# Kernel tuning notes

Hardware: AMD Instinct MI355X
Metric: run time of the kernel (lower is better)

## Reference

```python
import jax, jax.numpy as jnp
import numpy as np

U, I, D = 100000, 100000, 64
B, T = 16384, 1_638_400
R = 5  # rating levels 1..5


def setup_inputs() -> dict:
    key = jax.random.key(0)
    ks = jax.random.split(key, 8)
    return {
        "user_idx": jax.random.randint(ks[0], (B,), 0, U, dtype=jnp.int32),
        "item_idx": jax.random.randint(ks[1], (B,), 0, I, dtype=jnp.int32),
        "flat_items": jax.random.randint(ks[2], (T,), 0, I, dtype=jnp.int32),
        "seg_ids": jnp.sort(jax.random.randint(ks[3], (T,), 0, B * R, dtype=jnp.int32)),
        "user_emb": (jax.random.uniform(ks[4], (U, D), dtype=jnp.float32) - 0.5) * 0.01,
        "item_emb": (jax.random.uniform(ks[5], (I, D), dtype=jnp.float32) - 0.5) * 0.01,
        "Mr": (jax.random.uniform(ks[6], (I, D), dtype=jnp.float32) - 0.5) * 0.01,
        "user_bias": jnp.zeros((U,), dtype=jnp.float32),
        "item_bias": jnp.zeros((I,), dtype=jnp.float32),
        "global_avg": jnp.float32(3.5),
    }


def reference(user_idx, item_idx, flat_items, seg_ids, user_emb, item_emb, Mr, user_bias, item_bias, global_avg):
    num_seg = B * R  # segment = sample_i * 5 + (rating - 1)
    # Original torch code does Mr_ik(rate_dict).sum() -> scalar over ALL dims,
    # then broadcasts that scalar onto the latent_dim vector UuMpc[i].
    row_sum = Mr[flat_items].sum(axis=-1)  # [T] per-item full-row sum
    # Emulate `rate_dict.remove(item_idx[i])`: mask out the target item of this sample.
    match = flat_items == item_idx[seg_ids // R]  # [T]
    contrib = jnp.where(match, 0.0, row_sum)
    seg_sum = jax.ops.segment_sum(contrib, seg_ids, num_segments=num_seg)  # [B*5]
    cnt = jax.ops.segment_sum(jnp.where(match, 0.0, 1.0), seg_ids, num_segments=num_seg)
    per_seg = jnp.where(cnt > 0, seg_sum / jnp.sqrt(jnp.maximum(cnt, 1.0)), 0.0)
    uu_mpc = per_seg.reshape(B, R).sum(axis=-1)  # [B] scalar per sample
    user_vec = user_emb[user_idx] + uu_mpc[:, None]  # broadcast scalar over latent dim
    item_vec = item_emb[item_idx]
    rui = (user_vec * item_vec).sum(axis=-1) + user_bias[user_idx] + item_bias[item_idx] + global_avg
    return jnp.clip(rui, 1.0, 5.0)
```

## Files before the change

kernel.cpp:

```cpp
#include <hip/hip_runtime.h>

#define U_N 100000
#define I_N 100000
#define D_N 64
#define B_N 16384
#define T_N 1638400
#define R_N 5
#define NSEG (B_N * R_N)
#define CHUNK 16

__global__ void rowsum_kernel(const float* __restrict__ Mr, float* __restrict__ rowsum) {
    int wave = (blockIdx.x * blockDim.x + threadIdx.x) >> 6;
    int lane = threadIdx.x & 63;
    if (wave >= I_N) return;
    float v = Mr[(long)wave * D_N + lane];
    #pragma unroll
    for (int off = 32; off >= 1; off >>= 1) v += __shfl_xor(v, off, 64);
    if (lane == 0) rowsum[wave] = v;
}

__global__ void seg_kernel(const int* __restrict__ flat_items,
                           const int* __restrict__ seg_ids,
                           const int* __restrict__ item_idx,
                           const float* __restrict__ rowsum,
                           float* __restrict__ seg_sum,
                           int* __restrict__ seg_cnt) {
    int tid = blockIdx.x * blockDim.x + threadIdx.x;
    long base = (long)tid * CHUNK;
    if (base >= T_N) return;

    const int4* fi4 = (const int4*)(flat_items + base);
    const int4* si4 = (const int4*)(seg_ids + base);

    int cur_seg = -1;
    float acc = 0.f;
    int cnt = 0;

    #pragma unroll
    for (int c = 0; c < CHUNK / 4; ++c) {
        int4 fi = fi4[c];
        int4 si = si4[c];
        int f[4] = {fi.x, fi.y, fi.z, fi.w};
        int s[4] = {si.x, si.y, si.z, si.w};
        #pragma unroll
        for (int j = 0; j < 4; ++j) {
            int sg = s[j];
            if (sg != cur_seg) {
                if (cnt > 0) {
                    atomicAdd(&seg_sum[cur_seg], acc);
                    atomicAdd(&seg_cnt[cur_seg], cnt);
                }
                cur_seg = sg; acc = 0.f; cnt = 0;
            }
            int it = f[j];
            if (it != item_idx[sg / R_N]) {
                acc += rowsum[it];
                cnt += 1;
            }
        }
    }
    if (cnt > 0) {
        atomicAdd(&seg_sum[cur_seg], acc);
        atomicAdd(&seg_cnt[cur_seg], cnt);
    }
}

__global__ void final_kernel(const int* __restrict__ user_idx,
                             const int* __restrict__ item_idx,
                             const float* __restrict__ user_emb,
                             const float* __restrict__ item_emb,
                             const float* __restrict__ user_bias,
                             const float* __restrict__ item_bias,
                             const float* __restrict__ global_avg,
                             const float* __restrict__ seg_sum,
                             const int* __restrict__ seg_cnt,
                             float* __restrict__ out) {
    int wave = (blockIdx.x * blockDim.x + threadIdx.x) >> 6;
    int lane = threadIdx.x & 63;
    if (wave >= B_N) return;
    int u = user_idx[wave];
    int it = item_idx[wave];
    float ue = user_emb[(long)u * D_N + lane];
    float ie = item_emb[(long)it * D_N + lane];
    float dot = ue * ie;
    float isum = ie;
    #pragma unroll
    for (int off = 32; off >= 1; off >>= 1) {
        dot += __shfl_xor(dot, off, 64);
        isum += __shfl_xor(isum, off, 64);
    }
    if (lane == 0) {
        float uu = 0.f;
        #pragma unroll
        for (int r = 0; r < R_N; ++r) {
            int s = wave * R_N + r;
            int c = seg_cnt[s];
            if (c > 0) uu += seg_sum[s] / sqrtf((float)c);
        }
        float rui = dot + uu * isum + user_bias[u] + item_bias[it] + global_avg[0];
        rui = fminf(fmaxf(rui, 1.0f), 5.0f);
        out[wave] = rui;
    }
}

extern "C" void kernel_launch(void* const* d_in, const int* in_sizes, int n_in,
                              void* d_out, int out_size, void* d_ws, size_t ws_size,
                              hipStream_t stream) {
    const int*   user_idx   = (const int*)d_in[0];
    const int*   item_idx   = (const int*)d_in[1];
    const int*   flat_items = (const int*)d_in[2];
    const int*   seg_ids    = (const int*)d_in[3];
    const float* user_emb   = (const float*)d_in[4];
    const float* item_emb   = (const float*)d_in[5];
    const float* Mr         = (const float*)d_in[6];
    const float* user_bias  = (const float*)d_in[7];
    const float* item_bias  = (const float*)d_in[8];
    const float* global_avg = (const float*)d_in[9];
    float* out = (float*)d_out;

    float* rowsum  = (float*)d_ws;
    float* seg_sum = rowsum + I_N;
    int*   seg_cnt = (int*)(seg_sum + NSEG);

    hipMemsetAsync(seg_sum, 0, (size_t)NSEG * sizeof(float) * 2, stream);

    rowsum_kernel<<<(I_N * 64 + 255) / 256, 256, 0, stream>>>(Mr, rowsum);
    seg_kernel<<<(T_N / CHUNK + 255) / 256, 256, 0, stream>>>(
        flat_items, seg_ids, item_idx, rowsum, seg_sum, seg_cnt);
    final_kernel<<<(B_N * 64 + 255) / 256, 256, 0, stream>>>(
        user_idx, item_idx, user_emb, item_emb, user_bias, item_bias,
        global_avg, seg_sum, seg_cnt, out);
}
```

Baseline: 161.6 us.

## Fuse segment reduction into per-sample kernel using binary search over seg_ids

Replaces the global-atomic segment kernel, the memset and the separate final kernel with a single per-sample kernel. Each wave binary-searches the sorted seg_ids for its sample's range, accumulates the five rating buckets with LDS atomics, then computes the dot product and output directly. The row-sum kernel also switches to float4 loads with 16 threads per row. The change removes the memset, one launch and the global atomic traffic, at the cost of two dependent-latency binary searches per wave and LDS atomic contention on five slots.

```diff
diff --git a/kernel.cpp b/kernel.cpp
--- a/kernel.cpp
+++ b/kernel.cpp
@@ -6,100 +6,91 @@
 #define B_N 16384
 #define T_N 1638400
 #define R_N 5
-#define NSEG (B_N * R_N)
-#define CHUNK 16
 
 __global__ void rowsum_kernel(const float* __restrict__ Mr, float* __restrict__ rowsum) {
-    int wave = (blockIdx.x * blockDim.x + threadIdx.x) >> 6;
-    int lane = threadIdx.x & 63;
-    if (wave >= I_N) return;
-    float v = Mr[(long)wave * D_N + lane];
-    #pragma unroll
-    for (int off = 32; off >= 1; off >>= 1) v += __shfl_xor(v, off, 64);
-    if (lane == 0) rowsum[wave] = v;
+    int tid = blockIdx.x * blockDim.x + threadIdx.x;
+    int row = tid >> 4;
+    int sub = tid & 15;
+    if (row >= I_N) return;
+    const float4* p = (const float4*)(Mr + (long)row * D_N);
+    float4 v4 = p[sub];
+    float v = v4.x + v4.y + v4.z + v4.w;
+    v += __shfl_xor(v, 1);
+    v += __shfl_xor(v, 2);
+    v += __shfl_xor(v, 4);
+    v += __shfl_xor(v, 8);
+    if (sub == 0) rowsum[row] = v;
 }
 
-__global__ void seg_kernel(const int* __restrict__ flat_items,
-                           const int* __restrict__ seg_ids,
-                           const int* __restrict__ item_idx,
-                           const float* __restrict__ rowsum,
-                           float* __restrict__ seg_sum,
-                           int* __restrict__ seg_cnt) {
-    int tid = blockIdx.x * blockDim.x + threadIdx.x;
-    long base = (long)tid * CHUNK;
-    if (base >= T_N) return;
+__device__ __forceinline__ int lower_bound_i(const int* __restrict__ a, int n, int val) {
+    int lo = 0, hi = n;
+    while (lo < hi) {
+        int mid = (lo + hi) >> 1;
+        if (a[mid] < val) lo = mid + 1; else hi = mid;
+    }
+    return lo;
+}
 
-    const int4* fi4 = (const int4*)(flat_items + base);
-    const int4* si4 = (const int4*)(seg_ids + base);
+__global__ void sample_kernel(const int* __restrict__ user_idx,
+                              const int* __restrict__ item_idx,
+                              const int* __restrict__ flat_items,
+                              const int* __restrict__ seg_ids,
+                              const float* __restrict__ user_emb,
+                              const float* __restrict__ item_emb,
+                              const float* __restrict__ user_bias,
+                              const float* __restrict__ item_bias,
+                              const float* __restrict__ global_avg,
+                              const float* __restrict__ rowsum,
+                              float* __restrict__ out) {
+    __shared__ float s_sum[4][5];
+    __shared__ int   s_cnt[4][5];
 
-    int cur_seg = -1;
-    float acc = 0.f;
-    int cnt = 0;
+    int w    = threadIdx.x >> 6;
+    int lane = threadIdx.x & 63;
+    int b    = blockIdx.x * 4 + w;
+    if (b >= B_N) return;
 
-    #pragma unroll
-    for (int c = 0; c < CHUNK / 4; ++c) {
-        int4 fi = fi4[c];
-        int4 si = si4[c];
-        int f[4] = {fi.x, fi.y, fi.z, fi.w};
-        int s[4] = {si.x, si.y, si.z, si.w};
-        #pragma unroll
-        for (int j = 0; j < 4; ++j) {
-            int sg = s[j];
-            if (sg != cur_seg) {
-                if (cnt > 0) {
-                    atomicAdd(&seg_sum[cur_seg], acc);
-                    atomicAdd(&seg_cnt[cur_seg], cnt);
-                }
-                cur_seg = sg; acc = 0.f; cnt = 0;
-            }
-            int it = f[j];
-            if (it != item_idx[sg / R_N]) {
-                acc += rowsum[it];
-                cnt += 1;
-            }
+    if (lane < R_N) { s_sum[w][lane] = 0.f; s_cnt[w][lane] = 0; }
+    __syncthreads();
+
+    int lo = lower_bound_i(seg_ids, T_N, b * R_N);
+    int hi = lower_bound_i(seg_ids, T_N, b * R_N + R_N);
+    int target = item_idx[b];
+
+    for (int t = lo + lane; t < hi; t += 64) {
+        int sg = seg_ids[t];
+        int it = flat_items[t];
+        if (it != target) {
+            int r = sg - b * R_N;
+            atomicAdd(&s_sum[w][r], rowsum[it]);
+            atomicAdd(&s_cnt[w][r], 1);
         }
     }
-    if (cnt > 0) {
-        atomicAdd(&seg_sum[cur_seg], acc);
-        atomicAdd(&seg_cnt[cur_seg], cnt);
+    __syncthreads();
+
+    float uu = 0.f;
+    if (lane == 0) {
+        #pragma unroll
+        for (int r = 0; r < R_N; ++r) {
+            int c = s_cnt[w][r];
+            if (c > 0) uu += s_sum[w][r] / sqrtf((float)c);
+        }
     }
-}
 
-__global__ void final_kernel(const int* __restrict__ user_idx,
-                             const int* __restrict__ item_idx,
-                             const float* __restrict__ user_emb,
-                             const float* __restrict__ item_emb,
-                             const float* __restrict__ user_bias,
-                             const float* __restrict__ item_bias,
-                             const float* __restrict__ global_avg,
-                             const float* __restrict__ seg_sum,
-                             const int* __restrict__ seg_cnt,
-                             float* __restrict__ out) {
-    int wave = (blockIdx.x * blockDim.x + threadIdx.x) >> 6;
-    int lane = threadIdx.x & 63;
-    if (wave >= B_N) return;
-    int u = user_idx[wave];
-    int it = item_idx[wave];
+    int u = user_idx[b];
     float ue = user_emb[(long)u * D_N + lane];
-    float ie = item_emb[(long)it * D_N + lane];
+    float ie = item_emb[(long)target * D_N + lane];
     float dot = ue * ie;
     float isum = ie;
     #pragma unroll
     for (int off = 32; off >= 1; off >>= 1) {
-        dot += __shfl_xor(dot, off, 64);
-        isum += __shfl_xor(isum, off, 64);
+        dot  += __shfl_xor(dot, off);
+        isum += __shfl_xor(isum, off);
     }
     if (lane == 0) {
-        float uu = 0.f;
-        #pragma unroll
-        for (int r = 0; r < R_N; ++r) {
-            int s = wave * R_N + r;
-            int c = seg_cnt[s];
-            if (c > 0) uu += seg_sum[s] / sqrtf((float)c);
-        }
-        float rui = dot + uu * isum + user_bias[u] + item_bias[it] + global_avg[0];
+        float rui = dot + uu * isum + user_bias[u] + item_bias[target] + global_avg[0];
         rui = fminf(fmaxf(rui, 1.0f), 5.0f);
-        out[wave] = rui;
+        out[b] = rui;
     }
 }
 
@@ -118,16 +109,10 @@
     const float* global_avg = (const float*)d_in[9];
     float* out = (float*)d_out;
 
-    float* rowsum  = (float*)d_ws;
-    float* seg_sum = rowsum + I_N;
-    int*   seg_cnt = (int*)(seg_sum + NSEG);
+    float* rowsum = (float*)d_ws;
 
-    hipMemsetAsync(seg_sum, 0, (size_t)NSEG * sizeof(float) * 2, stream);
-
-    rowsum_kernel<<<(I_N * 64 + 255) / 256, 256, 0, stream>>>(Mr, rowsum);
-    seg_kernel<<<(T_N / CHUNK + 255) / 256, 256, 0, stream>>>(
-        flat_items, seg_ids, item_idx, rowsum, seg_sum, seg_cnt);
-    final_kernel<<<(B_N * 64 + 255) / 256, 256, 0, stream>>>(
-        user_idx, item_idx, user_emb, item_emb, user_bias, item_bias,
-        global_avg, seg_sum, seg_cnt, out);
+    rowsum_kernel<<<(I_N * 16 + 255) / 256, 256, 0, stream>>>(Mr, rowsum);
+    sample_kernel<<<B_N / 4, 256, 0, stream>>>(
+        user_idx, item_idx, flat_items, seg_ids, user_emb, item_emb,
+        user_bias, item_bias, global_avg, rowsum, out);
 }
```

After: 166.5 us. 1.03x slower.
